# Kernel tuning notes

Measured on AMD Instinct MI355X. Metric: run time of the kernel, lower is better.

Reference implementation:

```python
import jax, jax.numpy as jnp
import numpy as np
from jax import lax

N_FEATURES = 160
HIDDEN = 128
NUM_LAYERS = 2
BATCH = 256
SEQ = 512


def _lstm_layer(x, h0, c0, W_ih, W_hh, b_ih, b_hh):
    """Single LSTM layer, batch_first input x: [B, T, D]. Returns hs: [B, T, H].
    PyTorch gate order: i, f, g, o."""
    b = b_ih + b_hh  # [4H]

    def step(carry, xt):
        h, c = carry
        gates = xt @ W_ih.T + h @ W_hh.T + b  # [B, 4H]
        i, f, g, o = jnp.split(gates, 4, axis=-1)
        i = jax.nn.sigmoid(i)
        f = jax.nn.sigmoid(f)
        g = jnp.tanh(g)
        o = jax.nn.sigmoid(o)
        c = f * c + i * g
        h = o * jnp.tanh(c)
        return (h, c), h

    xs = jnp.swapaxes(x, 0, 1)  # [T, B, D]
    (_, _), hs = lax.scan(step, (h0, c0), xs)
    return jnp.swapaxes(hs, 0, 1)  # [B, T, H]


def setup_inputs() -> dict:
    key = jax.random.key(0)
    ks = jax.random.split(key, 9)
    s = 1.0 / np.sqrt(HIDDEN)  # PyTorch LSTM init scale
    x = jax.random.normal(ks[0], (BATCH, SEQ, N_FEATURES), dtype=jnp.float32)
    h0 = jnp.zeros((NUM_LAYERS, BATCH, HIDDEN), dtype=jnp.float32)
    c0 = jnp.zeros((NUM_LAYERS, BATCH, HIDDEN), dtype=jnp.float32)
    return {
        "x": x,
        "h0": h0,
        "c0": c0,
        "W_ih0": jax.random.uniform(ks[1], (4 * HIDDEN, N_FEATURES), jnp.float32, -s, s),
        "W_hh0": jax.random.uniform(ks[2], (4 * HIDDEN, HIDDEN), jnp.float32, -s, s),
        "b_ih0": jax.random.uniform(ks[3], (4 * HIDDEN,), jnp.float32, -s, s),
        "b_hh0": jax.random.uniform(ks[4], (4 * HIDDEN,), jnp.float32, -s, s),
        "W_ih1": jax.random.uniform(ks[5], (4 * HIDDEN, HIDDEN), jnp.float32, -s, s),
        "W_hh1": jax.random.uniform(ks[6], (4 * HIDDEN, HIDDEN), jnp.float32, -s, s),
        "b_ih1": jax.random.uniform(ks[7], (4 * HIDDEN,), jnp.float32, -s, s),
        "b_hh1": jax.random.uniform(ks[8], (4 * HIDDEN,), jnp.float32, -s, s),
    }


def reference(x, h0, c0, W_ih0, W_hh0, b_ih0, b_hh0, W_ih1, W_hh1, b_ih1, b_hh1):
    h1 = _lstm_layer(x, h0[0], c0[0], W_ih0, W_hh0, b_ih0, b_hh0)   # [B, T, H]
    h2 = _lstm_layer(h1, h0[1], c0[1], W_ih1, W_hh1, b_ih1, b_hh1)  # [B, T, H]
    return h2[:, -1:, :]  # [B, 1, H]
```

## Files before the change

### kernel.cpp

```cpp
#include <hip/hip_runtime.h>


typedef _Float16 f16;
typedef _Float16 f16x8 __attribute__((ext_vector_type(8)));
typedef float f32x4 __attribute__((ext_vector_type(4)));

#define B_  256
#define T_  512
#define HID 128
#define NG  512
#define KX0 160
#define NC  4
#define TC  128

static __device__ __forceinline__ unsigned pack2(float a, float b) {
  union { f16 h[2]; unsigned u; } v;
  v.h[0] = (f16)a; v.h[1] = (f16)b;
  return v.u;
}

static __device__ __forceinline__ float dot2f(unsigned a, unsigned b, float c) {
  float d;
  asm("v_dot2_f32_f16 %0, %1, %2, %3" : "=v"(d) : "v"(a), "v"(b), "v"(c));
  return d;
}

static __device__ __forceinline__ float fast_rcp(float x) {
#if __has_builtin(__builtin_amdgcn_rcpf)
  return __builtin_amdgcn_rcpf(x);
#else
  return 1.0f / x;
#endif
}
static __device__ __forceinline__ float fast_exp2(float x) {
#if __has_builtin(__builtin_amdgcn_exp2f)
  return __builtin_amdgcn_exp2f(x);
#else
  return exp2f(x);
#endif
}
static __device__ __forceinline__ float sigm(float x) {
  return fast_rcp(1.0f + fast_exp2(x * -1.44269504f));
}
static __device__ __forceinline__ float tanh_f(float x) {
  float e = fast_exp2(x * 2.885390082f);
  return 1.0f - 2.0f * fast_rcp(e + 1.0f);
}

template <int CTRL>
static __device__ __forceinline__ float qp_add(float v) {
  int iv = __builtin_bit_cast(int, v);
  int t = __builtin_amdgcn_update_dpp(iv, iv, CTRL, 0xF, 0xF, true);
  return v + __builtin_bit_cast(float, t);
}

static __device__ __forceinline__ float gxval(const uint4& g, int j) {
  unsigned w = (j >> 1) == 0 ? g.x : (j >> 1) == 1 ? g.y : (j >> 1) == 2 ? g.z : g.w;
  unsigned hs = (j & 1) ? (w >> 16) : (w & 0xffffu);
  f16 v = __builtin_bit_cast(f16, (unsigned short)hs);
  return (float)v;
}

template <int K, bool AF16>
__global__ __launch_bounds__(256) void gemm_xw(
    const void* __restrict__ Aptr, size_t bStride,
    const float* __restrict__ W, f16* __restrict__ D) {
  constexpr int KP = K + 8;
  __shared__ f16 As[128][KP];
  __shared__ f16 Bs[64][KP];
  const int tid = threadIdx.x;
  const int mtile = blockIdx.x, ntile = blockIdx.y;

  if (AF16) {
    const f16* A = (const f16*)Aptr;
    for (int i = tid; i < 128 * (K / 8); i += 256) {
      int r = i / (K / 8), kk = (i % (K / 8)) * 8;
      size_t grow = (size_t)mtile * 128 + r;
      uint4 v = *(const uint4*)(A + grow * K + kk);
      *(uint4*)&As[r][kk] = v;
    }
  } else {
    const float* A = (const float*)Aptr;
    for (int i = tid; i < 128 * (K / 4); i += 256) {
      int r = i / (K / 4), kk = (i % (K / 4)) * 4;
      int grow = mtile * 128 + r;
      int bb = grow >> 7, tt = grow & (TC - 1);
      const float* p = A + (size_t)bb * bStride + (size_t)tt * K + kk;
      float4 v = *(const float4*)p;
      uint2 u;
      u.x = pack2(v.x, v.y);
      u.y = pack2(v.z, v.w);
      *(uint2*)&As[r][kk] = u;
    }
  }
  for (int i = tid; i < 64 * (K / 4); i += 256) {
    int r = i / (K / 4), kk = (i % (K / 4)) * 4;
    const float* p = W + (size_t)(ntile * 64 + r) * K + kk;
    float4 v = *(const float4*)p;
    uint2 u;
    u.x = pack2(v.x, v.y);
    u.y = pack2(v.z, v.w);
    *(uint2*)&Bs[r][kk] = u;
  }
  __syncthreads();

  const int w = tid >> 6, l = tid & 63;
  const int lr = l & 15, lg = l >> 4;
  f32x4 acc[2][4] = {};
#pragma unroll
  for (int ks = 0; ks < K / 32; ++ks) {
    f16x8 a0 = *(const f16x8*)&As[w * 32 + lr][ks * 32 + lg * 8];
    f16x8 a1 = *(const f16x8*)&As[w * 32 + 16 + lr][ks * 32 + lg * 8];
    f16x8 bf[4];
#pragma unroll
    for (int nj = 0; nj < 4; ++nj)
      bf[nj] = *(const f16x8*)&Bs[nj * 16 + lr][ks * 32 + lg * 8];
#pragma unroll
    for (int nj = 0; nj < 4; ++nj) {
      acc[0][nj] = __builtin_amdgcn_mfma_f32_16x16x32_f16(a0, bf[nj], acc[0][nj], 0, 0, 0);
      acc[1][nj] = __builtin_amdgcn_mfma_f32_16x16x32_f16(a1, bf[nj], acc[1][nj], 0, 0, 0);
    }
  }
#pragma unroll
  for (int mi = 0; mi < 2; ++mi) {
#pragma unroll
    for (int nj = 0; nj < 4; ++nj) {
      int col = ntile * 64 + nj * 16 + lr;
      int cell = col & 127, gate = col >> 7;
      int rowbase = mtile * 128 + w * 32 + mi * 16 + lg * 4;
      int bb = rowbase >> 7, tt = rowbase & (TC - 1);
      unsigned lo = pack2(acc[mi][nj][0], acc[mi][nj][1]);
      unsigned hi = pack2(acc[mi][nj][2], acc[mi][nj][3]);
      size_t idx = (((size_t)bb * HID + cell) * 4 + gate) * TC + tt;
      uint2 u; u.x = lo; u.y = hi;
      *(uint2*)(D + idx) = u;
    }
  }
}

struct RecArgs {
  const f16* Gx;
  const float* Whh;
  const float* bih; const float* bhh;
  const float* hin; const float* cin;
  float* hst; float* cst;
  f16* h1out;
  float* fin;
};

__global__ __launch_bounds__(512) void lstm_rec2(RecArgs A, RecArgs B, int nA) {
  const RecArgs& P = ((int)blockIdx.x < nA) ? A : B;
  const int b = ((int)blockIdx.x < nA) ? blockIdx.x : blockIdx.x - nA;
  const int tid = threadIdx.x;
  const int c = tid >> 2, s = tid & 3;
  __shared__ unsigned hbuf[2][64];

  unsigned wh[4][16];
  float bias[4];
#pragma unroll
  for (int g = 0; g < 4; ++g) {
    const int r = g * HID + c;
#pragma unroll
    for (int j = 0; j < 16; ++j) {
      int p = 16 * s + j;
      wh[g][j] = pack2(P.Whh[(size_t)r * HID + 2 * p], P.Whh[(size_t)r * HID + 2 * p + 1]);
    }
    bias[g] = P.bih[r] + P.bhh[r];
  }
  float cstate = P.cin[b * HID + c];
  if (tid < 64)
    hbuf[0][tid] = pack2(P.hin[b * HID + 2 * tid], P.hin[b * HID + 2 * tid + 1]);

  const f16* gxb = P.Gx + ((size_t)b * HID + c) * 4 * TC;
  f16* h1x = P.h1out ? P.h1out + (size_t)b * TC * HID + c : (f16*)nullptr;

  uint4 gA[4], gB[4];
#pragma unroll
  for (int g = 0; g < 4; ++g) gA[g] = *(const uint4*)(gxb + (size_t)g * TC + 0);
  __syncthreads();

  float hprev = 0.f;

  auto STEP = [&](const uint4 (&gx)[4], int t, int j) {
    if (h1x && s == 0 && t > 0) h1x[(size_t)(t - 1) * HID] = (f16)hprev;
    const uint4* hs4 = (const uint4*)&hbuf[t & 1][16 * s];
    float ai = 0.f, af = 0.f, ag = 0.f, ao = 0.f;
#pragma unroll
    for (int k = 0; k < 4; ++k) {
      uint4 v = hs4[k];
      ai = dot2f(v.x, wh[0][4 * k + 0], ai); ai = dot2f(v.y, wh[0][4 * k + 1], ai);
      ai = dot2f(v.z, wh[0][4 * k + 2], ai); ai = dot2f(v.w, wh[0][4 * k + 3], ai);
      af = dot2f(v.x, wh[1][4 * k + 0], af); af = dot2f(v.y, wh[1][4 * k + 1], af);
      af = dot2f(v.z, wh[1][4 * k + 2], af); af = dot2f(v.w, wh[1][4 * k + 3], af);
      ag = dot2f(v.x, wh[2][4 * k + 0], ag); ag = dot2f(v.y, wh[2][4 * k + 1], ag);
      ag = dot2f(v.z, wh[2][4 * k + 2], ag); ag = dot2f(v.w, wh[2][4 * k + 3], ag);
      ao = dot2f(v.x, wh[3][4 * k + 0], ao); ao = dot2f(v.y, wh[3][4 * k + 1], ao);
      ao = dot2f(v.z, wh[3][4 * k + 2], ao); ao = dot2f(v.w, wh[3][4 * k + 3], ao);
    }
    ai = qp_add<0xB1>(ai); ai = qp_add<0x4E>(ai);
    af = qp_add<0xB1>(af); af = qp_add<0x4E>(af);
    ag = qp_add<0xB1>(ag); ag = qp_add<0x4E>(ag);
    ao = qp_add<0xB1>(ao); ao = qp_add<0x4E>(ao);

    float iv = sigm(ai + bias[0] + gxval(gx[0], j));
    float fv = sigm(af + bias[1] + gxval(gx[1], j));
    float gv = tanh_f(ag + bias[2] + gxval(gx[2], j));
    float ov = sigm(ao + bias[3] + gxval(gx[3], j));
    cstate = fv * cstate + iv * gv;
    float h = ov * tanh_f(cstate);
    if (s == 0) ((f16*)&hbuf[(t + 1) & 1][0])[c] = (f16)h;
    hprev = h;
    __syncthreads();
  };

#pragma unroll 1
  for (int t0 = 0; t0 < TC; t0 += 16) {
    {
      int tn = t0 + 8;
#pragma unroll
      for (int g = 0; g < 4; ++g) gB[g] = *(const uint4*)(gxb + (size_t)g * TC + tn);
    }
#pragma unroll
    for (int j = 0; j < 8; ++j) STEP(gA, t0 + j, j);
    {
      int tm = t0 + 16; if (tm > TC - 8) tm = TC - 8;
#pragma unroll
      for (int g = 0; g < 4; ++g) gA[g] = *(const uint4*)(gxb + (size_t)g * TC + tm);
    }
#pragma unroll
    for (int j = 0; j < 8; ++j) STEP(gB, t0 + 8 + j, j);
  }

  if (h1x && s == 0) h1x[(size_t)(TC - 1) * HID] = (f16)hprev;
  if (s == 0) {
    P.hst[b * HID + c] = (float)(f16)hprev;
    P.cst[b * HID + c] = cstate;
    if (P.fin) P.fin[b * HID + c] = hprev;
  }
}

extern "C" void kernel_launch(void* const* d_in, const int* in_sizes, int n_in,
                              void* d_out, int out_size, void* d_ws,
                              size_t ws_size, hipStream_t stream) {
  const float* x    = (const float*)d_in[0];
  const float* h0   = (const float*)d_in[1];
  const float* c0   = (const float*)d_in[2];
  const float* Wih0 = (const float*)d_in[3];
  const float* Whh0 = (const float*)d_in[4];
  const float* bih0 = (const float*)d_in[5];
  const float* bhh0 = (const float*)d_in[6];
  const float* Wih1 = (const float*)d_in[7];
  const float* Whh1 = (const float*)d_in[8];
  const float* bih1 = (const float*)d_in[9];
  const float* bhh1 = (const float*)d_in[10];

  char* w = (char*)d_ws;
  f16* Gx0 = (f16*)w;      w += (size_t)B_ * TC * NG * 2;
  f16* Gx1 = (f16*)w;      w += (size_t)B_ * TC * NG * 2;
  f16* h1  = (f16*)w;      w += (size_t)B_ * TC * HID * 2;
  float* sH0 = (float*)w;  w += (size_t)B_ * HID * 4;
  float* sC0 = (float*)w;  w += (size_t)B_ * HID * 4;
  float* sH1 = (float*)w;  w += (size_t)B_ * HID * 4;
  float* sC1 = (float*)w;

  const dim3 ggrid(B_ * TC / 128, 8);

  auto l0args = [&](int cc) {
    RecArgs a;
    a.Gx = Gx0; a.Whh = Whh0; a.bih = bih0; a.bhh = bhh0;
    a.hin = cc == 0 ? h0 : sH0; a.cin = cc == 0 ? c0 : sC0;
    a.hst = sH0; a.cst = sC0; a.h1out = h1; a.fin = nullptr;
    return a;
  };
  auto l1args = [&](int cc) {
    RecArgs a;
    a.Gx = Gx1; a.Whh = Whh1; a.bih = bih1; a.bhh = bhh1;
    a.hin = cc == 0 ? h0 + B_ * HID : sH1; a.cin = cc == 0 ? c0 + B_ * HID : sC1;
    a.hst = sH1; a.cst = sC1; a.h1out = nullptr;
    a.fin = cc == NC - 1 ? (float*)d_out : nullptr;
    return a;
  };

  RecArgs dummy = {};

  gemm_xw<KX0, false><<<ggrid, 256, 0, stream>>>(
      x + (size_t)0 * TC * KX0, (size_t)T_ * KX0, Wih0, Gx0);
  lstm_rec2<<<B_, 512, 0, stream>>>(l0args(0), dummy, B_);

  for (int cc = 1; cc < NC; ++cc) {
    gemm_xw<HID, true><<<ggrid, 256, 0, stream>>>(h1, 0, Wih1, Gx1);
    gemm_xw<KX0, false><<<ggrid, 256, 0, stream>>>(
        x + (size_t)cc * TC * KX0, (size_t)T_ * KX0, Wih0, Gx0);
    lstm_rec2<<<2 * B_, 512, 0, stream>>>(l0args(cc), l1args(cc - 1), B_);
  }

  gemm_xw<HID, true><<<ggrid, 256, 0, stream>>>(h1, 0, Wih1, Gx1);
  lstm_rec2<<<B_, 512, 0, stream>>>(l1args(NC - 1), dummy, B_);
}
```

Baseline: 909.7 us.

## Halve threads per LSTM cell, fold biases into input GEMM, simplify prefetch

The recurrent kernel now uses 2 threads per hidden cell (256 threads per block) instead of 4, with each thread holding 32 packed weight words per gate. This halves the cross-lane reduction to a single DPP step and cuts block-wide barrier cost. Biases are added in the input-projection GEMM epilogue instead of per step in the recurrence. The double-buffered Gx prefetch is replaced by a plain per-8-step load, which may expose global-load latency and raises per-thread register pressure and serial dot-product length.

Result: faster. 886.1 us (-2.6%).

```diff
diff --git a/kernel.cpp b/kernel.cpp
--- a/kernel.cpp
+++ b/kernel.cpp
@@ -47,10 +47,9 @@
   return 1.0f - 2.0f * fast_rcp(e + 1.0f);
 }
 
-template <int CTRL>
-static __device__ __forceinline__ float qp_add(float v) {
+static __device__ __forceinline__ float qp_add1(float v) {
   int iv = __builtin_bit_cast(int, v);
-  int t = __builtin_amdgcn_update_dpp(iv, iv, CTRL, 0xF, 0xF, true);
+  int t = __builtin_amdgcn_update_dpp(iv, iv, 0xB1, 0xF, 0xF, true);
   return v + __builtin_bit_cast(float, t);
 }
 
@@ -64,7 +63,9 @@
 template <int K, bool AF16>
 __global__ __launch_bounds__(256) void gemm_xw(
     const void* __restrict__ Aptr, size_t bStride,
-    const float* __restrict__ W, f16* __restrict__ D) {
+    const float* __restrict__ W,
+    const float* __restrict__ bihp, const float* __restrict__ bhhp,
+    f16* __restrict__ D) {
   constexpr int KP = K + 8;
   __shared__ f16 As[128][KP];
   __shared__ f16 Bs[64][KP];
@@ -126,11 +127,12 @@
 #pragma unroll
     for (int nj = 0; nj < 4; ++nj) {
       int col = ntile * 64 + nj * 16 + lr;
+      float bsum = bihp[col] + bhhp[col];
       int cell = col & 127, gate = col >> 7;
       int rowbase = mtile * 128 + w * 32 + mi * 16 + lg * 4;
       int bb = rowbase >> 7, tt = rowbase & (TC - 1);
-      unsigned lo = pack2(acc[mi][nj][0], acc[mi][nj][1]);
-      unsigned hi = pack2(acc[mi][nj][2], acc[mi][nj][3]);
+      unsigned lo = pack2(acc[mi][nj][0] + bsum, acc[mi][nj][1] + bsum);
+      unsigned hi = pack2(acc[mi][nj][2] + bsum, acc[mi][nj][3] + bsum);
       size_t idx = (((size_t)bb * HID + cell) * 4 + gate) * TC + tt;
       uint2 u; u.x = lo; u.y = hi;
       *(uint2*)(D + idx) = u;
@@ -141,31 +143,28 @@
 struct RecArgs {
   const f16* Gx;
   const float* Whh;
-  const float* bih; const float* bhh;
   const float* hin; const float* cin;
   float* hst; float* cst;
   f16* h1out;
   float* fin;
 };
 
-__global__ __launch_bounds__(512) void lstm_rec2(RecArgs A, RecArgs B, int nA) {
+__global__ __launch_bounds__(256) void lstm_rec2(RecArgs A, RecArgs B, int nA) {
   const RecArgs& P = ((int)blockIdx.x < nA) ? A : B;
   const int b = ((int)blockIdx.x < nA) ? blockIdx.x : blockIdx.x - nA;
   const int tid = threadIdx.x;
-  const int c = tid >> 2, s = tid & 3;
+  const int c = tid >> 1, s = tid & 1;
   __shared__ unsigned hbuf[2][64];
 
-  unsigned wh[4][16];
-  float bias[4];
+  unsigned wh[4][32];
 #pragma unroll
   for (int g = 0; g < 4; ++g) {
     const int r = g * HID + c;
 #pragma unroll
-    for (int j = 0; j < 16; ++j) {
-      int p = 16 * s + j;
+    for (int j = 0; j < 32; ++j) {
+      int p = 32 * s + j;
       wh[g][j] = pack2(P.Whh[(size_t)r * HID + 2 * p], P.Whh[(size_t)r * HID + 2 * p + 1]);
     }
-    bias[g] = P.bih[r] + P.bhh[r];
   }
   float cstate = P.cin[b * HID + c];
   if (tid < 64)
@@ -173,62 +172,46 @@
 
   const f16* gxb = P.Gx + ((size_t)b * HID + c) * 4 * TC;
   f16* h1x = P.h1out ? P.h1out + (size_t)b * TC * HID + c : (f16*)nullptr;
-
-  uint4 gA[4], gB[4];
-#pragma unroll
-  for (int g = 0; g < 4; ++g) gA[g] = *(const uint4*)(gxb + (size_t)g * TC + 0);
   __syncthreads();
 
   float hprev = 0.f;
 
-  auto STEP = [&](const uint4 (&gx)[4], int t, int j) {
-    if (h1x && s == 0 && t > 0) h1x[(size_t)(t - 1) * HID] = (f16)hprev;
-    const uint4* hs4 = (const uint4*)&hbuf[t & 1][16 * s];
-    float ai = 0.f, af = 0.f, ag = 0.f, ao = 0.f;
-#pragma unroll
-    for (int k = 0; k < 4; ++k) {
-      uint4 v = hs4[k];
-      ai = dot2f(v.x, wh[0][4 * k + 0], ai); ai = dot2f(v.y, wh[0][4 * k + 1], ai);
-      ai = dot2f(v.z, wh[0][4 * k + 2], ai); ai = dot2f(v.w, wh[0][4 * k + 3], ai);
-      af = dot2f(v.x, wh[1][4 * k + 0], af); af = dot2f(v.y, wh[1][4 * k + 1], af);
-      af = dot2f(v.z, wh[1][4 * k + 2], af); af = dot2f(v.w, wh[1][4 * k + 3], af);
-      ag = dot2f(v.x, wh[2][4 * k + 0], ag); ag = dot2f(v.y, wh[2][4 * k + 1], ag);
-      ag = dot2f(v.z, wh[2][4 * k + 2], ag); ag = dot2f(v.w, wh[2][4 * k + 3], ag);
-      ao = dot2f(v.x, wh[3][4 * k + 0], ao); ao = dot2f(v.y, wh[3][4 * k + 1], ao);
-      ao = dot2f(v.z, wh[3][4 * k + 2], ao); ao = dot2f(v.w, wh[3][4 * k + 3], ao);
-    }
-    ai = qp_add<0xB1>(ai); ai = qp_add<0x4E>(ai);
-    af = qp_add<0xB1>(af); af = qp_add<0x4E>(af);
-    ag = qp_add<0xB1>(ag); ag = qp_add<0x4E>(ag);
-    ao = qp_add<0xB1>(ao); ao = qp_add<0x4E>(ao);
-
-    float iv = sigm(ai + bias[0] + gxval(gx[0], j));
-    float fv = sigm(af + bias[1] + gxval(gx[1], j));
-    float gv = tanh_f(ag + bias[2] + gxval(gx[2], j));
-    float ov = sigm(ao + bias[3] + gxval(gx[3], j));
-    cstate = fv * cstate + iv * gv;
-    float h = ov * tanh_f(cstate);
-    if (s == 0) ((f16*)&hbuf[(t + 1) & 1][0])[c] = (f16)h;
-    hprev = h;
-    __syncthreads();
-  };
-
 #pragma unroll 1
-  for (int t0 = 0; t0 < TC; t0 += 16) {
-    {
-      int tn = t0 + 8;
-#pragma unroll
-      for (int g = 0; g < 4; ++g) gB[g] = *(const uint4*)(gxb + (size_t)g * TC + tn);
-    }
-#pragma unroll
-    for (int j = 0; j < 8; ++j) STEP(gA, t0 + j, j);
-    {
-      int tm = t0 + 16; if (tm > TC - 8) tm = TC - 8;
-#pragma unroll
-      for (int g = 0; g < 4; ++g) gA[g] = *(const uint4*)(gxb + (size_t)g * TC + tm);
-    }
-#pragma unroll
-    for (int j = 0; j < 8; ++j) STEP(gB, t0 + 8 + j, j);
+  for (int t0 = 0; t0 < TC; t0 += 8) {
+    uint4 g4[4];
+#pragma unroll
+    for (int g = 0; g < 4; ++g) g4[g] = *(const uint4*)(gxb + (size_t)g * TC + t0);
+
+#pragma unroll
+    for (int j = 0; j < 8; ++j) {
+      const int t = t0 + j;
+      if (h1x && s == 0 && (j > 0 || t0 > 0)) h1x[(size_t)(t - 1) * HID] = (f16)hprev;
+      const uint4* hs4 = (const uint4*)&hbuf[t & 1][32 * s];
+      float ai = 0.f, af = 0.f, ag = 0.f, ao = 0.f;
+#pragma unroll
+      for (int k = 0; k < 8; ++k) {
+        uint4 v = hs4[k];
+        ai = dot2f(v.x, wh[0][4 * k + 0], ai); ai = dot2f(v.y, wh[0][4 * k + 1], ai);
+        ai = dot2f(v.z, wh[0][4 * k + 2], ai); ai = dot2f(v.w, wh[0][4 * k + 3], ai);
+        af = dot2f(v.x, wh[1][4 * k + 0], af); af = dot2f(v.y, wh[1][4 * k + 1], af);
+        af = dot2f(v.z, wh[1][4 * k + 2], af); af = dot2f(v.w, wh[1][4 * k + 3], af);
+        ag = dot2f(v.x, wh[2][4 * k + 0], ag); ag = dot2f(v.y, wh[2][4 * k + 1], ag);
+        ag = dot2f(v.z, wh[2][4 * k + 2], ag); ag = dot2f(v.w, wh[2][4 * k + 3], ag);
+        ao = dot2f(v.x, wh[3][4 * k + 0], ao); ao = dot2f(v.y, wh[3][4 * k + 1], ao);
+        ao = dot2f(v.z, wh[3][4 * k + 2], ao); ao = dot2f(v.w, wh[3][4 * k + 3], ao);
+      }
+      ai = qp_add1(ai); af = qp_add1(af); ag = qp_add1(ag); ao = qp_add1(ao);
+
+      float iv = sigm(ai + gxval(g4[0], j));
+      float fv = sigm(af + gxval(g4[1], j));
+      float gv = tanh_f(ag + gxval(g4[2], j));
+      float ov = sigm(ao + gxval(g4[3], j));
+      cstate = fv * cstate + iv * gv;
+      float h = ov * tanh_f(cstate);
+      if (s == 0) ((f16*)&hbuf[(t + 1) & 1][0])[c] = (f16)h;
+      hprev = h;
+      __syncthreads();
+    }
   }
 
   if (h1x && s == 0) h1x[(size_t)(TC - 1) * HID] = (f16)hprev;
@@ -267,14 +250,14 @@
 
   auto l0args = [&](int cc) {
     RecArgs a;
-    a.Gx = Gx0; a.Whh = Whh0; a.bih = bih0; a.bhh = bhh0;
+    a.Gx = Gx0; a.Whh = Whh0;
     a.hin = cc == 0 ? h0 : sH0; a.cin = cc == 0 ? c0 : sC0;
     a.hst = sH0; a.cst = sC0; a.h1out = h1; a.fin = nullptr;
     return a;
   };
   auto l1args = [&](int cc) {
     RecArgs a;
-    a.Gx = Gx1; a.Whh = Whh1; a.bih = bih1; a.bhh = bhh1;
+    a.Gx = Gx1; a.Whh = Whh1;
     a.hin = cc == 0 ? h0 + B_ * HID : sH1; a.cin = cc == 0 ? c0 + B_ * HID : sC1;
     a.hst = sH1; a.cst = sC1; a.h1out = nullptr;
     a.fin = cc == NC - 1 ? (float*)d_out : nullptr;
@@ -284,16 +267,16 @@
   RecArgs dummy = {};
 
   gemm_xw<KX0, false><<<ggrid, 256, 0, stream>>>(
-      x + (size_t)0 * TC * KX0, (size_t)T_ * KX0, Wih0, Gx0);
-  lstm_rec2<<<B_, 512, 0, stream>>>(l0args(0), dummy, B_);
+      x + (size_t)0 * TC * KX0, (size_t)T_ * KX0, Wih0, bih0, bhh0, Gx0);
+  lstm_rec2<<<B_, 256, 0, stream>>>(l0args(0), dummy, B_);
 
   for (int cc = 1; cc < NC; ++cc) {
-    gemm_xw<HID, true><<<ggrid, 256, 0, stream>>>(h1, 0, Wih1, Gx1);
+    gemm_xw<HID, true><<<ggrid, 256, 0, stream>>>(h1, 0, Wih1, bih1, bhh1, Gx1);
     gemm_xw<KX0, false><<<ggrid, 256, 0, stream>>>(
-        x + (size_t)cc * TC * KX0, (size_t)T_ * KX0, Wih0, Gx0);
-    lstm_rec2<<<2 * B_, 512, 0, stream>>>(l0args(cc), l1args(cc - 1), B_);
-  }
-
-  gemm_xw<HID, true><<<ggrid, 256, 0, stream>>>(h1, 0, Wih1, Gx1);
-  lstm_rec2<<<B_, 512, 0, stream>>>(l1args(NC - 1), dummy, B_);
-}
+        x + (size_t)cc * TC * KX0, (size_t)T_ * KX0, Wih0, bih0, bhh0, Gx0);
+    lstm_rec2<<<2 * B_, 256, 0, stream>>>(l0args(cc), l1args(cc - 1), B_);
+  }
+
+  gemm_xw<HID, true><<<ggrid, 256, 0, stream>>>(h1, 0, Wih1, bih1, bhh1, Gx1);
+  lstm_rec2<<<B_, 256, 0, stream>>>(l1args(NC - 1), dummy, B_);
+}
```
